# Performance work log

Hardware: AMD Instinct MI355X
Metric: run time of the kernel (lower is better)

Reference implementation:

```python
import jax, jax.numpy as jnp
import numpy as np

QUERY_DIM = 768
KEY_DIM = 1024


def setup_inputs() -> dict:
    key = jax.random.key(0)
    ks = jax.random.split(key, 8)
    B, LQ, LK = 16, 2048, 2048
    s_q = 1.0 / np.sqrt(QUERY_DIM)
    s_k = 1.0 / np.sqrt(KEY_DIM)
    return {
        "query": jax.random.normal(ks[0], (B, LQ, QUERY_DIM), jnp.float32),
        "key": jax.random.normal(ks[1], (B, LK, KEY_DIM), jnp.float32),
        "Wq": jax.random.uniform(ks[2], (QUERY_DIM, KEY_DIM), jnp.float32, -s_q, s_q),
        "bq": jax.random.uniform(ks[3], (KEY_DIM,), jnp.float32, -s_q, s_q),
        "Wk": jax.random.uniform(ks[4], (KEY_DIM, KEY_DIM), jnp.float32, -s_k, s_k),
        "bk": jax.random.uniform(ks[5], (KEY_DIM,), jnp.float32, -s_k, s_k),
        "Wv": jax.random.uniform(ks[6], (KEY_DIM, KEY_DIM), jnp.float32, -s_k, s_k),
        "bv": jax.random.uniform(ks[7], (KEY_DIM,), jnp.float32, -s_k, s_k),
    }


def reference(query, key, Wq, bq, Wk, bk, Wv, bv):
    # Linear projections (single-head)
    q = jnp.einsum('bqd,dk->bqk', query, Wq) + bq  # [B, Lq, Dk]
    k = jnp.einsum('bsd,dk->bsk', key, Wk) + bk    # [B, Lk, Dk]
    v = jnp.einsum('bsd,dk->bsk', key, Wv) + bv    # [B, Lk, Dk]
    d_k = k.shape[-1]
    scores = jnp.einsum('bqk,bsk->bqs', q, k) / jnp.sqrt(jnp.asarray(d_k, q.dtype))
    weights = jax.nn.softmax(scores, axis=-1)      # [B, Lq, Lk]
    return jnp.einsum('bqs,bsk->bqk', weights, v)  # [B, Lq, Dk]
```

## Files before the change

kernel.cpp:

```cpp
#include <hip/hip_runtime.h>
#include <hip/hip_bf16.h>


typedef __attribute__((ext_vector_type(4))) float  f32x4;
typedef __attribute__((ext_vector_type(8))) __bf16 bf16x8;

#define BM 128
#define BN 128
#define BK 32

__device__ __forceinline__ void gload_lds16(const __bf16* g, __bf16* l) {
    __builtin_amdgcn_global_load_lds(
        (const __attribute__((address_space(1))) void*)g,
        (__attribute__((address_space(3))) void*)l, 16, 0, 0);
}

enum { MODE_PROJ = 0, MODE_PROJT = 1, MODE_SCORE = 2, MODE_PV = 3 };

template <int MODE>
__global__ __launch_bounds__(256) void gemm128(
    const __bf16* __restrict__ Ag, const __bf16* __restrict__ Bg,
    const float* __restrict__ aux,
    float* __restrict__ rs,
    void* __restrict__ Cg,
    int K, int lda, int ldb, int ldc,
    long batchA, long batchB, long batchC, long batchRS)
{
    __shared__ __bf16 As[BM * BK];
    __shared__ __bf16 Bs[BN * BK];
    const int t    = threadIdx.x;
    const int lane = t & 63;
    const int w    = t >> 6;
    const int quad = lane >> 4;
    const int l15  = lane & 15;
    const int wm   = w >> 1, wn = w & 1;
    const int m0   = blockIdx.x * BM;
    const int n0   = blockIdx.y * BN;
    const int z    = blockIdx.z;

    const __bf16* A = Ag + (long)z * batchA;
    const __bf16* B = Bg + (long)z * batchB;

    const int srow = lane >> 2;
    const int scol = (lane & 3) * 8;

    f32x4 acc[4][4];
    #pragma unroll
    for (int jm = 0; jm < 4; ++jm)
        #pragma unroll
        for (int jn = 0; jn < 4; ++jn) acc[jm][jn] = (f32x4)(0.0f);

    for (int k0 = 0; k0 < K; k0 += BK) {
        #pragma unroll
        for (int i = 0; i < 2; ++i) {
            const int seg = w * 2 + i;
            gload_lds16(A + (long)(m0 + seg * 16 + srow) * lda + (k0 + scol),
                        As + seg * 512);
            gload_lds16(B + (long)(n0 + seg * 16 + srow) * ldb + (k0 + scol),
                        Bs + seg * 512);
        }
        __syncthreads();
        bf16x8 af[4], bfr[4];
        #pragma unroll
        for (int j = 0; j < 4; ++j) {
            af[j]  = *(const bf16x8*)&As[(wm * 64 + j * 16 + l15) * BK + quad * 8];
            bfr[j] = *(const bf16x8*)&Bs[(wn * 64 + j * 16 + l15) * BK + quad * 8];
        }
        #pragma unroll
        for (int jm = 0; jm < 4; ++jm)
            #pragma unroll
            for (int jn = 0; jn < 4; ++jn)
                acc[jm][jn] = __builtin_amdgcn_mfma_f32_16x16x32_bf16(
                    af[jm], bfr[jn], acc[jm][jn], 0, 0, 0);
        __syncthreads();
    }

    const int rowbase = m0 + wm * 64;
    const int colbase = n0 + wn * 64;

    if constexpr (MODE == MODE_PROJ) {
        __bf16* C = (__bf16*)Cg;
        #pragma unroll
        for (int jn = 0; jn < 4; ++jn) {
            const int col = colbase + jn * 16 + l15;
            const float bv = aux[col];
            #pragma unroll
            for (int jm = 0; jm < 4; ++jm)
                #pragma unroll
                for (int r = 0; r < 4; ++r) {
                    const int row = rowbase + jm * 16 + quad * 4 + r;
                    C[(long)row * ldc + col] = (__bf16)(acc[jm][jn][r] + bv);
                }
        }
    } else if constexpr (MODE == MODE_PROJT) {
        __bf16* C = (__bf16*)Cg;
        #pragma unroll
        for (int jm = 0; jm < 4; ++jm)
            #pragma unroll
            for (int r = 0; r < 4; ++r) {
                const int row = rowbase + jm * 16 + quad * 4 + r;
                const float bv = aux[row];
                #pragma unroll
                for (int jn = 0; jn < 4; ++jn) {
                    const int col = colbase + jn * 16 + l15;
                    C[(long)row * ldc + col] = (__bf16)(acc[jm][jn][r] + bv);
                }
            }
    } else if constexpr (MODE == MODE_SCORE) {
        const float sc = 0.03125f * 1.44269504088896f;
        __bf16* C = (__bf16*)Cg + (long)z * batchC;
        float* rsz = rs + (long)z * batchRS;
        #pragma unroll
        for (int jm = 0; jm < 4; ++jm) {
            float s[4] = {0.f, 0.f, 0.f, 0.f};
            #pragma unroll
            for (int jn = 0; jn < 4; ++jn) {
                const int col = colbase + jn * 16 + l15;
                #pragma unroll
                for (int r = 0; r < 4; ++r) {
                    const int row = rowbase + jm * 16 + quad * 4 + r;
                    const float e = exp2f(acc[jm][jn][r] * sc);
                    C[(long)row * ldc + col] = (__bf16)e;
                    s[r] += e;
                }
            }
            #pragma unroll
            for (int r = 0; r < 4; ++r) {
                float v = s[r];
                v += __shfl_xor(v, 1);
                v += __shfl_xor(v, 2);
                v += __shfl_xor(v, 4);
                v += __shfl_xor(v, 8);
                if (l15 == 0)
                    atomicAdd(&rsz[rowbase + jm * 16 + quad * 4 + r], v);
            }
        }
    } else {
        float* C = (float*)Cg + (long)z * batchC;
        const float* rsz = rs + (long)z * batchRS;
        #pragma unroll
        for (int jm = 0; jm < 4; ++jm) {
            float inv[4];
            #pragma unroll
            for (int r = 0; r < 4; ++r)
                inv[r] = 1.0f / rsz[rowbase + jm * 16 + quad * 4 + r];
            #pragma unroll
            for (int jn = 0; jn < 4; ++jn) {
                const int col = colbase + jn * 16 + l15;
                #pragma unroll
                for (int r = 0; r < 4; ++r) {
                    const int row = rowbase + jm * 16 + quad * 4 + r;
                    C[(long)row * ldc + col] = acc[jm][jn][r] * inv[r];
                }
            }
        }
    }
}

__global__ __launch_bounds__(256) void conv_bf16(const float* __restrict__ in,
                                                 __bf16* __restrict__ out, long n8)
{
    const long stride = (long)gridDim.x * blockDim.x;
    for (long i = (long)blockIdx.x * blockDim.x + threadIdx.x; i < n8; i += stride) {
        const float4* p = (const float4*)(in + i * 8);
        const float4 a = p[0], b = p[1];
        bf16x8 o;
        o[0] = (__bf16)a.x; o[1] = (__bf16)a.y; o[2] = (__bf16)a.z; o[3] = (__bf16)a.w;
        o[4] = (__bf16)b.x; o[5] = (__bf16)b.y; o[6] = (__bf16)b.z; o[7] = (__bf16)b.w;
        *(bf16x8*)(out + i * 8) = o;
    }
}

__global__ __launch_bounds__(256) void transpose_w(const float* __restrict__ W,
                                                   __bf16* __restrict__ WT,
                                                   int K, int N)
{
    __shared__ float tile[32][33];
    const int n0 = blockIdx.x * 32, k0 = blockIdx.y * 32;
    const int c = threadIdx.x & 31, r4 = threadIdx.x >> 5;
    #pragma unroll
    for (int i = 0; i < 4; ++i) {
        const int r = r4 + i * 8;
        tile[r][c] = W[(long)(k0 + r) * N + n0 + c];
    }
    __syncthreads();
    #pragma unroll
    for (int i = 0; i < 4; ++i) {
        const int r = r4 + i * 8;
        WT[(long)(n0 + r) * K + k0 + c] = (__bf16)tile[c][r];
    }
}

extern "C" void kernel_launch(void* const* d_in, const int* in_sizes, int n_in,
                              void* d_out, int out_size, void* d_ws, size_t ws_size,
                              hipStream_t stream) {
    const float* query = (const float*)d_in[0];
    const float* key   = (const float*)d_in[1];
    const float* Wq    = (const float*)d_in[2];
    const float* bq    = (const float*)d_in[3];
    const float* Wk    = (const float*)d_in[4];
    const float* bk    = (const float*)d_in[5];
    const float* Wv    = (const float*)d_in[6];
    const float* bv    = (const float*)d_in[7];
    float* out = (float*)d_out;

    const int B = 16, Lq = 2048, Lk = 2048, Dq = 768, Dk = 1024;
    const long M = (long)B * Lq;

    char* base = (char*)d_ws;
    __bf16* P   = (__bf16*)base;
    __bf16* qa  = (__bf16*)base;
    __bf16* ka  = (__bf16*)(base + 50331648);
    __bf16* WqT = (__bf16*)(base + 117440512);
    __bf16* WkT = (__bf16*)(base + 119013376);
    __bf16* WvT = (__bf16*)(base + 121110528);
    char* p2 = base + 134217728;
    __bf16* q  = (__bf16*)p2;  p2 += M * Dk * 2;
    __bf16* k  = (__bf16*)p2;  p2 += M * Dk * 2;
    __bf16* vT = (__bf16*)p2;  p2 += M * Dk * 2;
    float* row_sum = (float*)p2; p2 += M * 4;
    if ((size_t)(p2 - base) > ws_size) return;

    dim3 blk(256);

    conv_bf16<<<512, blk, 0, stream>>>(query, qa, M * Dq / 8);
    conv_bf16<<<512, blk, 0, stream>>>(key,   ka, M * Dk / 8);
    transpose_w<<<dim3(Dk / 32, Dq / 32), blk, 0, stream>>>(Wq, WqT, Dq, Dk);
    transpose_w<<<dim3(Dk / 32, Dk / 32), blk, 0, stream>>>(Wk, WkT, Dk, Dk);
    transpose_w<<<dim3(Dk / 32, Dk / 32), blk, 0, stream>>>(Wv, WvT, Dk, Dk);
    hipMemsetAsync(row_sum, 0, M * 4, stream);

    gemm128<MODE_PROJ><<<dim3(M / BM, Dk / BN, 1), blk, 0, stream>>>(
        qa, WqT, bq, nullptr, q, Dq, Dq, Dq, Dk, 0, 0, 0, 0);
    gemm128<MODE_PROJ><<<dim3(M / BM, Dk / BN, 1), blk, 0, stream>>>(
        ka, WkT, bk, nullptr, k, Dk, Dk, Dk, Dk, 0, 0, 0, 0);
    gemm128<MODE_PROJT><<<dim3(Dk / BM, M / BN, 1), blk, 0, stream>>>(
        WvT, ka, bv, nullptr, vT, Dk, Dk, Dk, (int)M, 0, 0, 0, 0);

    gemm128<MODE_SCORE><<<dim3(Lq / BM, Lk / BN, B), blk, 0, stream>>>(
        q, k, nullptr, row_sum, P, Dk, Dk, Dk, Lk,
        (long)Lq * Dk, (long)Lk * Dk, (long)Lq * Lk, Lq);

    gemm128<MODE_PV><<<dim3(Lq / BM, Dk / BN, B), blk, 0, stream>>>(
        P, vT, nullptr, row_sum, out, Lk, Lk, (int)M, Dk,
        (long)Lq * Lk, (long)Lk, (long)Lq * Dk, Lq);
}
```

Measured before the change: 1.107 ms.

## Double K tile with XOR-swizzled LDS and batch-contiguous V transpose layout

```diff
diff --git a/kernel.cpp b/kernel.cpp
--- a/kernel.cpp
+++ b/kernel.cpp
@@ -7,7 +7,7 @@
 
 #define BM 128
 #define BN 128
-#define BK 32
+#define BK 64
 
 __device__ __forceinline__ void gload_lds16(const __bf16* g, __bf16* l) {
     __builtin_amdgcn_global_load_lds(
@@ -16,6 +16,10 @@
 }
 
 enum { MODE_PROJ = 0, MODE_PROJT = 1, MODE_SCORE = 2, MODE_PV = 3 };
+
+__device__ __forceinline__ int lds_off(int R, int kc) {
+    return R * BK + ((kc ^ (R & 7)) * 8);
+}
 
 template <int MODE>
 __global__ __launch_bounds__(256) void gemm128(
@@ -41,8 +45,17 @@
     const __bf16* A = Ag + (long)z * batchA;
     const __bf16* B = Bg + (long)z * batchB;
 
-    const int srow = lane >> 2;
-    const int scol = (lane & 3) * 8;
+    const int srow = lane >> 3;
+    const int kcs  = ((lane & 7) ^ srow) * 8;
+
+    const __bf16* ap[4];
+    const __bf16* bp[4];
+    #pragma unroll
+    for (int i = 0; i < 4; ++i) {
+        const int seg = w * 4 + i;
+        ap[i] = A + (long)(m0 + seg * 8 + srow) * lda + kcs;
+        bp[i] = B + (long)(n0 + seg * 8 + srow) * ldb + kcs;
+    }
 
     f32x4 acc[4][4];
     #pragma unroll
@@ -52,26 +65,32 @@
 
     for (int k0 = 0; k0 < K; k0 += BK) {
         #pragma unroll
-        for (int i = 0; i < 2; ++i) {
-            const int seg = w * 2 + i;
-            gload_lds16(A + (long)(m0 + seg * 16 + srow) * lda + (k0 + scol),
-                        As + seg * 512);
-            gload_lds16(B + (long)(n0 + seg * 16 + srow) * ldb + (k0 + scol),
-                        Bs + seg * 512);
+        for (int i = 0; i < 4; ++i) {
+            const int seg = w * 4 + i;
+            gload_lds16(ap[i], As + seg * 512);
+            gload_lds16(bp[i], Bs + seg * 512);
+            ap[i] += BK;
+            bp[i] += BK;
         }
         __syncthreads();
-        bf16x8 af[4], bfr[4];
-        #pragma unroll
-        for (int j = 0; j < 4; ++j) {
-            af[j]  = *(const bf16x8*)&As[(wm * 64 + j * 16 + l15) * BK + quad * 8];
-            bfr[j] = *(const bf16x8*)&Bs[(wn * 64 + j * 16 + l15) * BK + quad * 8];
-        }
-        #pragma unroll
-        for (int jm = 0; jm < 4; ++jm)
-            #pragma unroll
-            for (int jn = 0; jn < 4; ++jn)
-                acc[jm][jn] = __builtin_amdgcn_mfma_f32_16x16x32_bf16(
-                    af[jm], bfr[jn], acc[jm][jn], 0, 0, 0);
+        #pragma unroll
+        for (int kh = 0; kh < 2; ++kh) {
+            bf16x8 af[4], bfr[4];
+            #pragma unroll
+            for (int j = 0; j < 4; ++j) {
+                const int Ra = wm * 64 + j * 16 + l15;
+                const int Rb = wn * 64 + j * 16 + l15;
+                const int kc = kh * 4 + quad;
+                af[j]  = *(const bf16x8*)&As[lds_off(Ra, kc)];
+                bfr[j] = *(const bf16x8*)&Bs[lds_off(Rb, kc)];
+            }
+            #pragma unroll
+            for (int jm = 0; jm < 4; ++jm)
+                #pragma unroll
+                for (int jn = 0; jn < 4; ++jn)
+                    acc[jm][jn] = __builtin_amdgcn_mfma_f32_16x16x32_bf16(
+                        af[jm], bfr[jn], acc[jm][jn], 0, 0, 0);
+        }
         __syncthreads();
     }
 
@@ -103,7 +122,9 @@
                 #pragma unroll
                 for (int jn = 0; jn < 4; ++jn) {
                     const int col = colbase + jn * 16 + l15;
-                    C[(long)row * ldc + col] = (__bf16)(acc[jm][jn][r] + bv);
+                    const long idx = (long)(col >> 11) * (1024L * 2048)
+                                   + (long)row * 2048 + (col & 2047);
+                    C[idx] = (__bf16)(acc[jm][jn][r] + bv);
                 }
             }
     } else if constexpr (MODE == MODE_SCORE) {
@@ -235,13 +256,13 @@
     gemm128<MODE_PROJ><<<dim3(M / BM, Dk / BN, 1), blk, 0, stream>>>(
         ka, WkT, bk, nullptr, k, Dk, Dk, Dk, Dk, 0, 0, 0, 0);
     gemm128<MODE_PROJT><<<dim3(Dk / BM, M / BN, 1), blk, 0, stream>>>(
-        WvT, ka, bv, nullptr, vT, Dk, Dk, Dk, (int)M, 0, 0, 0, 0);
+        WvT, ka, bv, nullptr, vT, Dk, Dk, Dk, 0, 0, 0, 0, 0);
 
     gemm128<MODE_SCORE><<<dim3(Lq / BM, Lk / BN, B), blk, 0, stream>>>(
         q, k, nullptr, row_sum, P, Dk, Dk, Dk, Lk,
         (long)Lq * Dk, (long)Lk * Dk, (long)Lq * Lk, Lq);
 
     gemm128<MODE_PV><<<dim3(Lq / BM, Dk / BN, B), blk, 0, stream>>>(
-        P, vT, nullptr, row_sum, out, Lk, Lk, (int)M, Dk,
-        (long)Lq * Lk, (long)Lk, (long)Lq * Dk, Lq);
-}
+        P, vT, nullptr, row_sum, out, Lk, Lk, 2048, Dk,
+        (long)Lq * Lk, 1024L * 2048, (long)Lq * Dk, Lq);
+}
```

New measurement: 993.4 us. -10.2%, faster.
